# Performance work log

Measured on AMD Instinct MI355X. Metric: run time of the kernel, lower is better.

Reference implementation:

```python
import jax, jax.numpy as jnp
import numpy as np

NUM_EMBEDDING = 8192
EMBEDDING_DIM = 512
BS = 16384
NEG_SLOPE = 0.01  # torch LeakyReLU default


def setup_inputs() -> dict:
    key = jax.random.key(0)
    k1, k2, k3, k4, k5, k6, k7 = jax.random.split(key, 7)
    d, K = EMBEDDING_DIM, NUM_EMBEDDING
    s1 = 1.0 / np.sqrt(d)
    return {
        "encoded_eeg": jax.random.normal(k1, (BS, d), dtype=jnp.float32),
        "encoded_mel": jax.random.normal(k2, (BS, d), dtype=jnp.float32),
        "embeddings": jax.random.normal(k3, (K, d), dtype=jnp.float32),
        "W1": jax.random.uniform(k4, (d, d), jnp.float32, -s1, s1),
        "b1": jax.random.uniform(k5, (d,), jnp.float32, -s1, s1),
        "W2": jax.random.uniform(k6, (K, d), jnp.float32, -s1, s1),
        "b2": jax.random.uniform(k7, (K,), jnp.float32, -s1, s1),
    }


def reference(encoded_eeg, encoded_mel, embeddings, W1, b1, W2, b2):
    # --- nearest-codebook indices for mel (detached in original) ---
    flat_mel = encoded_mel.reshape(-1, EMBEDDING_DIM)
    dists = (jnp.sum(embeddings ** 2, axis=1)[None, :]
             + jnp.sum(flat_mel ** 2, axis=1, keepdims=True)
             - 2.0 * flat_mel @ embeddings.T)  # [BS, K]
    mel_indices = jnp.argmin(dists, axis=-1)  # [BS]

    # --- small MLP logits over eeg ---
    flat_eeg = encoded_eeg.reshape(-1, EMBEDDING_DIM)
    h = flat_eeg @ W1.T + b1
    h = jnp.where(h >= 0, h, NEG_SLOPE * h)  # LeakyReLU
    logits = h @ W2.T + b2  # [BS, K]

    eeg_indices = jnp.argmax(logits, axis=-1)
    acc_rate = jnp.mean((eeg_indices == mel_indices).astype(jnp.float32))

    # cross entropy (mean over batch)
    logp = jax.nn.log_softmax(logits, axis=-1)
    loss = -jnp.mean(jnp.take_along_axis(logp, mel_indices[:, None], axis=1))
    return (loss, acc_rate)
```

## Files before the change

### kernel.cpp

```cpp
#include <hip/hip_runtime.h>
#include <hip/hip_bf16.h>
#include <hip/hip_fp8.h>

#define BSZ 16384
#define DIM 512
#define NEMB 8192
#define NEG 0.01f
#define NSPLIT 8

typedef __attribute__((ext_vector_type(8))) short short8;
typedef __attribute__((ext_vector_type(4))) float f32x4;
typedef __attribute__((ext_vector_type(4))) int i32x4;
typedef __attribute__((ext_vector_type(8))) int i32x8;

typedef const __attribute__((address_space(1))) void GVT;
typedef __attribute__((address_space(3))) void LVT;

__device__ __forceinline__ void gl_lds16(const void* g, void* l) {
    __builtin_amdgcn_global_load_lds((GVT*)g, (LVT*)l, 16, 0, 0);
}

__device__ __forceinline__ float bf2f(unsigned short u) {
    union { unsigned int i; float f; } c; c.i = ((unsigned int)u) << 16; return c.f;
}
__device__ __forceinline__ unsigned short f2bf(float f) {
    union { __hip_bfloat16 h; unsigned short u; } c; c.h = __float2bfloat16(f); return c.u;
}
__device__ __forceinline__ unsigned char f2fp8(float f) {
    __hip_fp8_e4m3 t(f); return (unsigned char)t.__x;
}
__device__ __forceinline__ unsigned int fkey(float f) {
    unsigned int u = __float_as_uint(f);
    return u ^ ((unsigned int)((int)u >> 31) | 0x80000000u);
}

__device__ __forceinline__ size_t pack_addr(int r, int k) {
    int kg = k >> 6, ko = k & 63;
    int half = ko >> 5, lq = (ko & 31) >> 3, sub = ko & 7;
    int L = lq * 16 + (r & 15);
    return ((size_t)((r >> 4) * 8 + kg) << 10) + (size_t)(L << 4) + (half << 3) + sub;
}

__device__ __forceinline__ void vm4_barrier() {
    asm volatile("s_waitcnt vmcnt(4) lgkmcnt(0)\ns_barrier" ::: "memory");
}
__device__ __forceinline__ void vm0_barrier() {
    asm volatile("s_waitcnt vmcnt(0) lgkmcnt(0)\ns_barrier" ::: "memory");
}
__device__ __forceinline__ void lgkm_barrier() {
    asm volatile("s_waitcnt lgkmcnt(0)\ns_barrier" ::: "memory");
}

#define ISSUE_NT(NT, BUF) do { \
    const unsigned char* src_ = gB0p + (size_t)(NT) * 16384; \
    _Pragma("unroll") for (int i_ = 0; i_ < 4; i_++) \
        gl_lds16(src_ + i_ * 1024, &sB8[BUF][uWd + i_ * 1024]); \
} while (0)

#define LOADH(F0, F1, CUR, KP) do { \
    const unsigned char* lb_ = &sB8[CUR][(2 * (KP)) * 1024] + (lane << 4); \
    i32x4 a0_ = *(const i32x4*)lb_; \
    i32x4 a1_ = *(const i32x4*)(lb_ + 1024); \
    i32x4 b0_ = *(const i32x4*)(lb_ + 8192); \
    i32x4 b1_ = *(const i32x4*)(lb_ + 8192 + 1024); \
    F0 = __builtin_shufflevector(a0_, a1_, 0, 1, 2, 3, 4, 5, 6, 7); \
    F1 = __builtin_shufflevector(b0_, b1_, 0, 1, 2, 3, 4, 5, 6, 7); \
} while (0)

#define MFMA4(F0, F1, KP, FIRST) do { \
    __builtin_amdgcn_s_setprio(1); \
    _Pragma("unroll") for (int mi = 0; mi < 2; mi++) { \
        f32x4 c0_ = (FIRST) ? Z4 : acc[mi][0]; \
        f32x4 c1_ = (FIRST) ? Z4 : acc[mi][1]; \
        acc[mi][0] = __builtin_amdgcn_mfma_scale_f32_16x16x128_f8f6f4( \
            fa8[mi][KP], F0, c0_, 0, 0, 0, 0x7F7F7F7Fu, 0, 0x7F7F7F7Fu); \
        acc[mi][1] = __builtin_amdgcn_mfma_scale_f32_16x16x128_f8f6f4( \
            fa8[mi][KP], F1, c1_, 0, 0, 0, 0x7F7F7F7Fu, 0, 0x7F7F7F7Fu); \
    } \
    __builtin_amdgcn_s_setprio(0); \
} while (0)

#define COMPUTE(CUR) do { \
    LOADH(fB0, fB1, CUR, 0);  MFMA4(fB0, fB1, 0, 1); \
    LOADH(fB0, fB1, CUR, 1);  MFMA4(fB0, fB1, 1, 0); \
    LOADH(fB0, fB1, CUR, 2);  MFMA4(fB0, fB1, 2, 0); \
    LOADH(fB0, fB1, CUR, 3);  MFMA4(fB0, fB1, 3, 0); \
} while (0)

#define EPILOGUE(NT) do { \
    int j0 = ((NT) << 5) + l15; \
    if (is_logits) { \
        float bb0 = sAux[j0], bb1 = sAux[j0 + 16]; \
        unsigned int ic0 = (unsigned int)(NEMB - 1 - (nbase + j0)); \
        _Pragma("unroll") for (int mi = 0; mi < 2; mi++) \
            _Pragma("unroll") for (int rg = 0; rg < 4; rg++) { \
                float v0 = acc[mi][0][rg] + bb0; \
                float v1 = acc[mi][1][rg] + bb1; \
                int r = mi * 4 + rg; \
                s[r] += __expf(v0) + __expf(v1); \
                float m = fmaxf(v0, v1); \
                unsigned int ii = v1 > v0 ? ic0 - 16 : ic0; \
                unsigned int pk = (fkey(m) & 0xFFFFE000u) | ii; \
                pbest[r] = pbest[r] > pk ? pbest[r] : pk; \
            } \
    } else { \
        float en0 = sAux[j0], en1 = sAux[j0 + 16]; \
        unsigned int cl0 = (unsigned int)(nbase + j0); \
        _Pragma("unroll") for (int mi = 0; mi < 2; mi++) \
            _Pragma("unroll") for (int rg = 0; rg < 4; rg++) { \
                float v0 = fmaf(-2.f, acc[mi][0][rg], en0); \
                float v1 = fmaf(-2.f, acc[mi][1][rg], en1); \
                float m = fminf(v0, v1); \
                unsigned int ii = v1 < v0 ? cl0 + 16 : cl0; \
                unsigned int pk = (fkey(m) & 0xFFFFE000u) | ii; \
                int r = mi * 4 + rg; \
                pbest[r] = pbest[r] < pk ? pbest[r] : pk; \
            } \
    } \
} while (0)

__global__ void k_prep(const float* __restrict__ eeg, const float* __restrict__ mel,
                       const float* __restrict__ emb, const float* __restrict__ W2,
                       const float* __restrict__ W1,
                       unsigned short* __restrict__ o_eeg, unsigned short* __restrict__ o_w1,
                       unsigned char* __restrict__ o_mel8, unsigned char* __restrict__ o_emb8,
                       unsigned char* __restrict__ o_w28,
                       float* __restrict__ enorm,
                       float* __restrict__ acc2, int* __restrict__ cnt) {
    int bid = blockIdx.x, tid = threadIdx.x;
    if (bid == 0 && tid == 0) { acc2[0] = 0.f; acc2[1] = 0.f; *cnt = 0; }
    if (bid < 1024) {
        const int n_big = BSZ * DIM / 4;
        const int n_mid = NEMB * DIM / 4;
        const int n_w1  = DIM * DIM / 4;
        const int total = n_big * 2 + n_mid * 2 + n_w1;
        for (int i = bid * 256 + tid; i < total; i += 1024 * 256) {
            int j = i;
            if (j < n_big) {
                float4 v = ((const float4*)eeg)[j];
                ushort4 o; o.x = f2bf(v.x); o.y = f2bf(v.y); o.z = f2bf(v.z); o.w = f2bf(v.w);
                ((ushort4*)o_eeg)[j] = o;
            } else if ((j -= n_big) < n_w1) {
                float4 v = ((const float4*)W1)[j];
                ushort4 o; o.x = f2bf(v.x); o.y = f2bf(v.y); o.z = f2bf(v.z); o.w = f2bf(v.w);
                ((ushort4*)o_w1)[j] = o;
            } else if ((j -= n_w1) < n_big) {
                float4 v = ((const float4*)mel)[j];
                uchar4 o; o.x = f2fp8(v.x); o.y = f2fp8(v.y); o.z = f2fp8(v.z); o.w = f2fp8(v.w);
                *(uchar4*)(o_mel8 + pack_addr(j >> 7, (j & 127) * 4)) = o;
            } else if ((j -= n_big) < n_mid) {
                float4 v = ((const float4*)emb)[j];
                uchar4 o; o.x = f2fp8(v.x); o.y = f2fp8(v.y); o.z = f2fp8(v.z); o.w = f2fp8(v.w);
                *(uchar4*)(o_emb8 + pack_addr(j >> 7, (j & 127) * 4)) = o;
            } else {
                j -= n_mid;
                float4 v = ((const float4*)W2)[j];
                uchar4 o; o.x = f2fp8(v.x); o.y = f2fp8(v.y); o.z = f2fp8(v.z); o.w = f2fp8(v.w);
                *(uchar4*)(o_w28 + pack_addr(j >> 7, (j & 127) * 4)) = o;
            }
        }
    } else {
        int w = tid >> 6, lane = tid & 63;
        int row0 = (bid - 1024) * 8 + w * 2;
        #pragma unroll
        for (int t = 0; t < 2; t++) {
            int row = row0 + t;
            const float4* p = (const float4*)(emb + (size_t)row * DIM) + lane * 2;
            float4 a = p[0], b = p[1];
            float s = a.x*a.x + a.y*a.y + a.z*a.z + a.w*a.w
                    + b.x*b.x + b.y*b.y + b.z*b.z + b.w*b.w;
            #pragma unroll
            for (int d = 1; d < 64; d <<= 1) s += __shfl_xor(s, d);
            if (lane == 0) enorm[row] = s;
        }
    }
}

__launch_bounds__(256, 2)
__global__ void k_hgemm(const unsigned short* __restrict__ A,
                        const unsigned short* __restrict__ B,
                        const float* __restrict__ b1,
                        unsigned short* __restrict__ H,
                        unsigned char* __restrict__ H8) {
    __shared__ __align__(16) unsigned short sA[4096], sB[4096];
    int tid = threadIdx.x;
    int w = tid >> 6, lane = tid & 63;
    int wr = w >> 1, wc = w & 1;
    int lquad = lane >> 4, l15 = lane & 15;
    int mt = blockIdx.x >> 2, nt = blockIdx.x & 3;
    int m0 = mt * 128, n0 = nt * 128;

    int e0 = w * 512 + lane * 8;
    int r0 = e0 >> 5, ce = e0 & 31;
    const unsigned short* gA0 = A + (m0 + r0) * DIM + ce;
    const unsigned short* gA1 = gA0 + 64 * DIM;
    const unsigned short* gB0 = B + (n0 + r0) * DIM + ce;
    const unsigned short* gB1 = gB0 + 64 * DIM;
    unsigned short* lA0 = sA + w * 512;  unsigned short* lA1 = sA + (w + 4) * 512;
    unsigned short* lB0 = sB + w * 512;  unsigned short* lB1 = sB + (w + 4) * 512;

    int offA[4], offB[4];
    #pragma unroll
    for (int i = 0; i < 4; i++) {
        offA[i] = (wr * 64 + i * 16 + l15) * 32 + lquad * 8;
        offB[i] = (wc * 64 + i * 16 + l15) * 32 + lquad * 8;
    }

    f32x4 acc[4][4];
    #pragma unroll
    for (int mi = 0; mi < 4; mi++)
        #pragma unroll
        for (int ni = 0; ni < 4; ni++) acc[mi][ni] = 0;

    for (int kk = 0; kk < 16; kk++) {
        gl_lds16(gA0, lA0); gl_lds16(gA1, lA1);
        gl_lds16(gB0, lB0); gl_lds16(gB1, lB1);
        gA0 += 32; gA1 += 32; gB0 += 32; gB1 += 32;
        __syncthreads();
        short8 af[4], bf_[4];
        #pragma unroll
        for (int i = 0; i < 4; i++) {
            af[i]  = *(const short8*)&sA[offA[i]];
            bf_[i] = *(const short8*)&sB[offB[i]];
        }
        #pragma unroll
        for (int mi = 0; mi < 4; mi++)
            #pragma unroll
            for (int ni = 0; ni < 4; ni++)
                acc[mi][ni] = __builtin_amdgcn_mfma_f32_16x16x32_bf16(af[mi], bf_[ni], acc[mi][ni], 0, 0, 0);
        __syncthreads();
    }

    #pragma unroll
    for (int ni = 0; ni < 4; ni++) {
        int col = n0 + wc * 64 + ni * 16 + l15;
        float bv = b1[col];
        #pragma unroll
        for (int mi = 0; mi < 4; mi++) {
            int rowb = m0 + wr * 64 + mi * 16 + lquad * 4;
            #pragma unroll
            for (int rg = 0; rg < 4; rg++) {
                float v = acc[mi][ni][rg] + bv;
                v = v >= 0.f ? v : NEG * v;
                H[(rowb + rg) * DIM + col] = f2bf(v);
                H8[pack_addr(rowb + rg, col)] = f2fp8(v);
            }
        }
    }
}

__launch_bounds__(256, 3)
__global__ void k_big(const unsigned char* __restrict__ Mel8,
                      const unsigned char* __restrict__ Emb8,
                      const unsigned char* __restrict__ H8,
                      const unsigned char* __restrict__ W28,
                      const float* __restrict__ enorm,
                      const float* __restrict__ b2,
                      float* __restrict__ p_s,
                      unsigned int* __restrict__ p_pmax,
                      unsigned int* __restrict__ p_pmin) {
    __shared__ __align__(16) unsigned char sB8[2][16384];
    __shared__ float sAux[1024];
    int tid = threadIdx.x;
    int w = tid >> 6, lane = tid & 63;
    int lquad = lane >> 4, l15 = lane & 15;
    int bid = blockIdx.x;
    int split = bid & 7;
    int is_logits = (bid >> 3) & 1;
    int mt = bid >> 4;
    int m0 = mt * 128, nbase = split * (NEMB / NSPLIT);

    const unsigned char* gAb = (is_logits ? H8 : Mel8);
    const unsigned char* gBb = (is_logits ? W28 : Emb8);

    #pragma unroll
    for (int j = 0; j < 4; j++) {
        int c = tid + j * 256;
        sAux[c] = is_logits ? b2[nbase + c] : (enorm[nbase + c] - 512.0f);
    }

    i32x8 fa8[2][4];
    #pragma unroll
    for (int mi = 0; mi < 2; mi++)
        #pragma unroll
        for (int kp = 0; kp < 4; kp++) {
            const unsigned char* p = gAb
                + ((size_t)(((m0 >> 4) + 2 * w + mi) * 8 + 2 * kp) << 10) + lane * 16;
            i32x4 lo = *(const i32x4*)p;
            i32x4 hi = *(const i32x4*)(p + 1024);
            fa8[mi][kp] = __builtin_shufflevector(lo, hi, 0, 1, 2, 3, 4, 5, 6, 7);
        }

    int uWd = w * 4096;
    const unsigned char* gB0p = gBb + (size_t)nbase * 512 + uWd + lane * 16;

    __syncthreads();

    const f32x4 Z4 = {0.f, 0.f, 0.f, 0.f};
    f32x4 acc[2][2];
    i32x8 fB0, fB1;

    float s[8];
    unsigned int pbest[8];
    unsigned int pinit = is_logits ? 0u : 0xFFFFFFFFu;
    #pragma unroll
    for (int r = 0; r < 8; r++) { s[r] = 0.f; pbest[r] = pinit; }

    ISSUE_NT(0, 0);
    ISSUE_NT(1, 1);
    for (int nt = 0; nt < 32; nt++) {
        int cur = nt & 1;
        if (nt < 31) vm4_barrier(); else vm0_barrier();
        COMPUTE(cur);
        lgkm_barrier();
        if (nt + 2 < 32) ISSUE_NT(nt + 2, cur);
        EPILOGUE(nt);
    }

    if (is_logits) {
        #pragma unroll
        for (int r = 0; r < 8; r++)
            #pragma unroll
            for (int d = 1; d < 16; d <<= 1) {
                s[r] += __shfl_xor(s[r], d);
                unsigned int o = (unsigned int)__shfl_xor((int)pbest[r], d);
                pbest[r] = pbest[r] > o ? pbest[r] : o;
            }
        if (l15 == 0) {
            #pragma unroll
            for (int mi = 0; mi < 2; mi++)
                #pragma unroll
                for (int rg = 0; rg < 4; rg++) {
                    int row = w * 32 + mi * 16 + lquad * 4 + rg;
                    int pidx = split * BSZ + m0 + row;
                    p_s[pidx] = s[mi * 4 + rg];
                    p_pmax[pidx] = pbest[mi * 4 + rg];
                }
        }
    } else {
        #pragma unroll
        for (int r = 0; r < 8; r++)
            #pragma unroll
            for (int d = 1; d < 16; d <<= 1) {
                unsigned int o = (unsigned int)__shfl_xor((int)pbest[r], d);
                pbest[r] = pbest[r] < o ? pbest[r] : o;
            }
        if (l15 == 0) {
            #pragma unroll
            for (int mi = 0; mi < 2; mi++)
                #pragma unroll
                for (int rg = 0; rg < 4; rg++) {
                    int row = w * 32 + mi * 16 + lquad * 4 + rg;
                    p_pmin[split * BSZ + m0 + row] = pbest[mi * 4 + rg];
                }
        }
    }
}

__global__ void k_tail(const float* __restrict__ p_s, const unsigned int* __restrict__ p_pmax,
                       const unsigned int* __restrict__ p_pmin,
                       const unsigned short* __restrict__ H,
                       const float* __restrict__ W2,
                       const float* __restrict__ b2,
                       float* __restrict__ acc2, int* __restrict__ cnt,
                       float* __restrict__ out) {
    __shared__ int s_idx[64];
    __shared__ float s_l1[64], s_match[64];
    __shared__ float s_d[4];
    int bid = blockIdx.x, tid = threadIdx.x;
    int w = tid >> 6, lane = tid & 63;
    int rbase = bid * 64;

    if (tid < 64) {
        int r = rbase + tid;
        float S = 0.f; unsigned int PM = 0u, PN = 0xFFFFFFFFu;
        #pragma unroll
        for (int sp = 0; sp < NSPLIT; sp++) {
            S += p_s[sp * BSZ + r];
            unsigned int a = p_pmax[sp * BSZ + r];
            PM = PM > a ? PM : a;
            unsigned int b = p_pmin[sp * BSZ + r];
            PN = PN < b ? PN : b;
        }
        int eidx = (NEMB - 1) - (int)(PM & 0x1FFFu);
        int midx = (int)(PN & 0x1FFFu);
        s_idx[tid] = midx;
        s_l1[tid] = __logf(S) - b2[midx];
        s_match[tid] = (eidx == midx) ? 1.f : 0.f;
    }
    __syncthreads();

    float d0 = 0.f, d1 = 0.f;
    for (int j = 0; j < 16; j++) {
        int rr = w * 16 + j;
        int ridx = s_idx[rr];
        uint4 hv = *(const uint4*)(H + (size_t)(rbase + rr) * DIM + lane * 8);
        const float4* wp = (const float4*)(W2 + (size_t)ridx * DIM + lane * 8);
        float4 w0 = wp[0], w1 = wp[1];
        float p = bf2f((unsigned short)(hv.x & 0xffff)) * w0.x + bf2f((unsigned short)(hv.x >> 16)) * w0.y
                + bf2f((unsigned short)(hv.y & 0xffff)) * w0.z + bf2f((unsigned short)(hv.y >> 16)) * w0.w
                + bf2f((unsigned short)(hv.z & 0xffff)) * w1.x + bf2f((unsigned short)(hv.z >> 16)) * w1.y
                + bf2f((unsigned short)(hv.w & 0xffff)) * w1.z + bf2f((unsigned short)(hv.w >> 16)) * w1.w;
        if (j & 1) d1 += p; else d0 += p;
    }
    float ds = d0 + d1;
    #pragma unroll
    for (int d = 1; d < 64; d <<= 1) ds += __shfl_xor(ds, d);
    if (lane == 0) s_d[w] = ds;

    __syncthreads();
    for (int st = 32; st > 0; st >>= 1) {
        if (tid < st) { s_l1[tid] += s_l1[tid + st]; s_match[tid] += s_match[tid + st]; }
        __syncthreads();
    }
    if (tid == 0) {
        float loss_blk = s_l1[0] - (s_d[0] + s_d[1] + s_d[2] + s_d[3]);
        atomicAdd(&acc2[0], loss_blk * (1.0f / BSZ));
        atomicAdd(&acc2[1], s_match[0] * (1.0f / BSZ));
        __threadfence();
        if (atomicAdd(cnt, 1) == 255) {
            float L = atomicAdd(&acc2[0], 0.f);
            float M = atomicAdd(&acc2[1], 0.f);
            out[0] = L; out[1] = M;
        }
    }
}

extern "C" void kernel_launch(void* const* d_in, const int* in_sizes, int n_in,
                              void* d_out, int out_size, void* d_ws, size_t ws_size,
                              hipStream_t stream) {
    const float* eeg = (const float*)d_in[0];
    const float* mel = (const float*)d_in[1];
    const float* emb = (const float*)d_in[2];
    const float* W1  = (const float*)d_in[3];
    const float* b1  = (const float*)d_in[4];
    const float* W2  = (const float*)d_in[5];
    const float* b2  = (const float*)d_in[6];
    float* out = (float*)d_out;

    unsigned short* ws_eeg = (unsigned short*)d_ws;
    unsigned short* ws_w1  = ws_eeg + (size_t)BSZ * DIM;
    unsigned short* ws_h   = ws_w1  + (size_t)DIM * DIM;
    unsigned char*  ws_h8  = (unsigned char*)(ws_h + (size_t)BSZ * DIM);
    unsigned char*  ws_mel8 = ws_h8  + (size_t)BSZ * DIM;
    unsigned char*  ws_emb8 = ws_mel8 + (size_t)BSZ * DIM;
    unsigned char*  ws_w28  = ws_emb8 + (size_t)NEMB * DIM;
    float* ws_en  = (float*)(ws_w28 + (size_t)NEMB * DIM);
    float* p_s    = ws_en + NEMB;
    unsigned int* p_pmax = (unsigned int*)(p_s + (size_t)NSPLIT * BSZ);
    unsigned int* p_pmin = p_pmax + (size_t)NSPLIT * BSZ;
    float* acc2   = (float*)(p_pmin + (size_t)NSPLIT * BSZ);
    int*   cnt    = (int*)(acc2 + 2);

    k_prep<<<2048, 256, 0, stream>>>(eeg, mel, emb, W2, W1,
                                     ws_eeg, ws_w1, ws_mel8, ws_emb8, ws_w28,
                                     ws_en, acc2, cnt);
    k_hgemm<<<(BSZ / 128) * (DIM / 128), 256, 0, stream>>>(ws_eeg, ws_w1, b1, ws_h, ws_h8);
    k_big<<<(BSZ / 128) * NSPLIT * 2, 256, 0, stream>>>(ws_mel8, ws_emb8, ws_h8, ws_w28,
                                                        ws_en, b2, p_s, p_pmax, p_pmin);
    k_tail<<<BSZ / 64, 256, 0, stream>>>(p_s, p_pmax, p_pmin, ws_h, W2, b2, acc2, cnt, out);
}
```

Baseline: 326.8 us.

## Double-buffer B fragment loads in fp8 GEMM and fuse codebook norms into prep

The inner compute step of the main fp8 GEMM now uses two fragment register sets. The LDS read for the next k-slice is issued before the MFMAs that consume the previous slice, so LDS latency overlaps with matrix math. Separately, the codebook row-norm computation is folded into the fp8 conversion pass of the embeddings, using a wave shuffle plus a small shared-memory reduction. This removes a second read of the embedding table and halves the prep grid. The cost is extra VGPR pressure from the added fragment registers and block-wide barriers inside the embedding branch of the prep loop.

Result: no change. 325.8 us (-0.3%).

```diff
diff --git a/kernel.cpp b/kernel.cpp
--- a/kernel.cpp
+++ b/kernel.cpp
@@ -81,10 +81,14 @@
 } while (0)
 
 #define COMPUTE(CUR) do { \
-    LOADH(fB0, fB1, CUR, 0);  MFMA4(fB0, fB1, 0, 1); \
-    LOADH(fB0, fB1, CUR, 1);  MFMA4(fB0, fB1, 1, 0); \
-    LOADH(fB0, fB1, CUR, 2);  MFMA4(fB0, fB1, 2, 0); \
-    LOADH(fB0, fB1, CUR, 3);  MFMA4(fB0, fB1, 3, 0); \
+    LOADH(fA0, fA1, CUR, 0); \
+    LOADH(fB0, fB1, CUR, 1); \
+    MFMA4(fA0, fA1, 0, 1); \
+    LOADH(fA0, fA1, CUR, 2); \
+    MFMA4(fB0, fB1, 1, 0); \
+    LOADH(fB0, fB1, CUR, 3); \
+    MFMA4(fA0, fA1, 2, 0); \
+    MFMA4(fB0, fB1, 3, 0); \
 } while (0)
 
 #define EPILOGUE(NT) do { \
@@ -127,51 +131,45 @@
                        unsigned char* __restrict__ o_w28,
                        float* __restrict__ enorm,
                        float* __restrict__ acc2, int* __restrict__ cnt) {
+    __shared__ float sps[4];
     int bid = blockIdx.x, tid = threadIdx.x;
+    int w = tid >> 6, lane = tid & 63;
     if (bid == 0 && tid == 0) { acc2[0] = 0.f; acc2[1] = 0.f; *cnt = 0; }
-    if (bid < 1024) {
-        const int n_big = BSZ * DIM / 4;
-        const int n_mid = NEMB * DIM / 4;
-        const int n_w1  = DIM * DIM / 4;
-        const int total = n_big * 2 + n_mid * 2 + n_w1;
-        for (int i = bid * 256 + tid; i < total; i += 1024 * 256) {
-            int j = i;
-            if (j < n_big) {
-                float4 v = ((const float4*)eeg)[j];
-                ushort4 o; o.x = f2bf(v.x); o.y = f2bf(v.y); o.z = f2bf(v.z); o.w = f2bf(v.w);
-                ((ushort4*)o_eeg)[j] = o;
-            } else if ((j -= n_big) < n_w1) {
-                float4 v = ((const float4*)W1)[j];
-                ushort4 o; o.x = f2bf(v.x); o.y = f2bf(v.y); o.z = f2bf(v.z); o.w = f2bf(v.w);
-                ((ushort4*)o_w1)[j] = o;
-            } else if ((j -= n_w1) < n_big) {
-                float4 v = ((const float4*)mel)[j];
-                uchar4 o; o.x = f2fp8(v.x); o.y = f2fp8(v.y); o.z = f2fp8(v.z); o.w = f2fp8(v.w);
-                *(uchar4*)(o_mel8 + pack_addr(j >> 7, (j & 127) * 4)) = o;
-            } else if ((j -= n_big) < n_mid) {
-                float4 v = ((const float4*)emb)[j];
-                uchar4 o; o.x = f2fp8(v.x); o.y = f2fp8(v.y); o.z = f2fp8(v.z); o.w = f2fp8(v.w);
-                *(uchar4*)(o_emb8 + pack_addr(j >> 7, (j & 127) * 4)) = o;
-            } else {
-                j -= n_mid;
-                float4 v = ((const float4*)W2)[j];
-                uchar4 o; o.x = f2fp8(v.x); o.y = f2fp8(v.y); o.z = f2fp8(v.z); o.w = f2fp8(v.w);
-                *(uchar4*)(o_w28 + pack_addr(j >> 7, (j & 127) * 4)) = o;
-            }
-        }
-    } else {
-        int w = tid >> 6, lane = tid & 63;
-        int row0 = (bid - 1024) * 8 + w * 2;
-        #pragma unroll
-        for (int t = 0; t < 2; t++) {
-            int row = row0 + t;
-            const float4* p = (const float4*)(emb + (size_t)row * DIM) + lane * 2;
-            float4 a = p[0], b = p[1];
-            float s = a.x*a.x + a.y*a.y + a.z*a.z + a.w*a.w
-                    + b.x*b.x + b.y*b.y + b.z*b.z + b.w*b.w;
-            #pragma unroll
-            for (int d = 1; d < 64; d <<= 1) s += __shfl_xor(s, d);
-            if (lane == 0) enorm[row] = s;
+    const int n_big = BSZ * DIM / 4;
+    const int n_mid = NEMB * DIM / 4;
+    const int n_w1  = DIM * DIM / 4;
+    const int total = n_big * 2 + n_mid * 2 + n_w1;
+    for (int i = bid * 256 + tid; i < total; i += 1024 * 256) {
+        int j = i;
+        if (j < n_big) {
+            float4 v = ((const float4*)eeg)[j];
+            ushort4 o; o.x = f2bf(v.x); o.y = f2bf(v.y); o.z = f2bf(v.z); o.w = f2bf(v.w);
+            ((ushort4*)o_eeg)[j] = o;
+        } else if ((j -= n_big) < n_w1) {
+            float4 v = ((const float4*)W1)[j];
+            ushort4 o; o.x = f2bf(v.x); o.y = f2bf(v.y); o.z = f2bf(v.z); o.w = f2bf(v.w);
+            ((ushort4*)o_w1)[j] = o;
+        } else if ((j -= n_w1) < n_big) {
+            float4 v = ((const float4*)mel)[j];
+            uchar4 o; o.x = f2fp8(v.x); o.y = f2fp8(v.y); o.z = f2fp8(v.z); o.w = f2fp8(v.w);
+            *(uchar4*)(o_mel8 + pack_addr(j >> 7, (j & 127) * 4)) = o;
+        } else if ((j -= n_big) < n_mid) {
+            float4 v = ((const float4*)emb)[j];
+            uchar4 o; o.x = f2fp8(v.x); o.y = f2fp8(v.y); o.z = f2fp8(v.z); o.w = f2fp8(v.w);
+            *(uchar4*)(o_emb8 + pack_addr(j >> 7, (j & 127) * 4)) = o;
+            float ss = v.x*v.x + v.y*v.y + v.z*v.z + v.w*v.w;
+            #pragma unroll
+            for (int d = 1; d < 64; d <<= 1) ss += __shfl_xor(ss, d);
+            if (lane == 0) sps[w] = ss;
+            __syncthreads();
+            if (tid == 0)   enorm[j >> 7]       = sps[0] + sps[1];
+            if (tid == 128) enorm[(j >> 7)]     = sps[2] + sps[3];
+            __syncthreads();
+        } else {
+            j -= n_mid;
+            float4 v = ((const float4*)W2)[j];
+            uchar4 o; o.x = f2fp8(v.x); o.y = f2fp8(v.y); o.z = f2fp8(v.z); o.w = f2fp8(v.w);
+            *(uchar4*)(o_w28 + pack_addr(j >> 7, (j & 127) * 4)) = o;
         }
     }
 }
@@ -298,7 +296,7 @@
 
     const f32x4 Z4 = {0.f, 0.f, 0.f, 0.f};
     f32x4 acc[2][2];
-    i32x8 fB0, fB1;
+    i32x8 fA0, fA1, fB0, fB1;
 
     float s[8];
     unsigned int pbest[8];
@@ -452,7 +450,7 @@
     float* acc2   = (float*)(p_pmin + (size_t)NSPLIT * BSZ);
     int*   cnt    = (int*)(acc2 + 2);
 
-    k_prep<<<2048, 256, 0, stream>>>(eeg, mel, emb, W2, W1,
+    k_prep<<<1024, 256, 0, stream>>>(eeg, mel, emb, W2, W1,
                                      ws_eeg, ws_w1, ws_mel8, ws_emb8, ws_w28,
                                      ws_en, acc2, cnt);
     k_hgemm<<<(BSZ / 128) * (DIM / 128), 256, 0, stream>>>(ws_eeg, ws_w1, b1, ws_h, ws_h8);
```
